# Performance work log

Hardware: AMD Instinct MI355X
Metric: run time of the kernel (lower is better)

## Reference

```python
import jax, jax.numpy as jnp
import numpy as np


def _conv2d(x, w, b, pad, rhs_dilation=(1, 1)):
    out = jax.lax.conv_general_dilated(
        x, w, window_strides=(1, 1),
        padding=((pad, pad), (pad, pad)),
        rhs_dilation=rhs_dilation,
        dimension_numbers=('NCHW', 'OIHW', 'NCHW'))
    return out + b[None, :, None, None]


def _bilinear(img, gx, gy):
    # img [C,H,W]; gx,gy [9,h,w] in [-1,1]; grid_sample bilinear, align_corners=True.
    # Coords are pre-clamped to [-1,1] so all samples are in-bounds; clamped
    # neighbor indices get zero bilinear weight at the boundary, matching torch.
    C, H, W = img.shape
    ix = (gx + 1.0) * 0.5 * (W - 1)
    iy = (gy + 1.0) * 0.5 * (H - 1)
    x0 = jnp.floor(ix)
    y0 = jnp.floor(iy)
    wx = ix - x0
    wy = iy - y0
    x0i = jnp.clip(x0.astype(jnp.int32), 0, W - 1)
    x1i = jnp.clip(x0i + 1, 0, W - 1)
    y0i = jnp.clip(y0.astype(jnp.int32), 0, H - 1)
    y1i = jnp.clip(y0i + 1, 0, H - 1)
    v00 = img[:, y0i, x0i]
    v01 = img[:, y0i, x1i]
    v10 = img[:, y1i, x0i]
    v11 = img[:, y1i, x1i]
    return (v00 * (1 - wx) * (1 - wy) + v01 * wx * (1 - wy)
            + v10 * (1 - wx) * wy + v11 * wx * wy)  # [C,9,h,w]


def _forward(x, conv_w, conv_b, offset_w, offset_b, mod_w, mod_b):
    b, c, h, w = x.shape
    offset = _conv2d(x, offset_w, offset_b, pad=1)          # [b,18,h,w]
    gx = jnp.clip(offset[:, :9] + jnp.linspace(-1.0, 1.0, w)[None, None, None, :], -1.0, 1.0)
    gy = jnp.clip(offset[:, 9:] + jnp.linspace(-1.0, 1.0, h)[None, None, :, None], -1.0, 1.0)
    sampled = jax.vmap(_bilinear)(x, gx, gy)                # [b,c,9,h,w]
    mod = _conv2d(x, mod_w, mod_b, pad=1)                   # [b,9,h,w]
    interp = sampled * mod[:, None]                         # [b,c,9,h,w]
    # tile the 9 samples into a 3h x 3w spatial grid: sample k = i + j*3 goes to block (j, i)
    tiled = interp.reshape(b, c, 3, 3, h, w).transpose(0, 1, 2, 4, 3, 5).reshape(b, c, 3 * h, 3 * w)
    # dilated 3x3 conv with dilation (h+1, w+1), stride 1, padding 1 -> [b,oc,h,w]
    return _conv2d(tiled, conv_w, conv_b, pad=1, rhs_dilation=(h + 1, w + 1))


def setup_inputs() -> dict:
    key = jax.random.key(0)
    ks = jax.random.split(key, 7)
    B, C, OC, H, W = 8, 256, 256, 64, 64
    return {
        'x': jax.random.normal(ks[0], (B, C, H, W), jnp.float32),
        'conv_w': jax.random.normal(ks[1], (OC, C, 3, 3), jnp.float32) * 0.02,
        'conv_b': jax.random.normal(ks[2], (OC,), jnp.float32) * 0.02,
        'offset_w': jax.random.normal(ks[3], (18, C, 3, 3), jnp.float32) * 0.01,
        'offset_b': jax.random.normal(ks[4], (18,), jnp.float32) * 0.01,
        'mod_w': jax.random.normal(ks[5], (9, C, 3, 3), jnp.float32) * 0.02,
        'mod_b': jax.random.normal(ks[6], (9,), jnp.float32) * 0.02,
    }


def reference(x, conv_w, conv_b, offset_w, offset_b, mod_w, mod_b):
    return _forward(x, conv_w, conv_b, offset_w, offset_b, mod_w, mod_b)
```

## Files before the change

### kernel.cpp

```cpp
#include <hip/hip_runtime.h>

typedef __attribute__((ext_vector_type(8))) _Float16 f16x8;
typedef __attribute__((ext_vector_type(4))) float f32x4;

#define CB 8
#define CC 256
#define CHW 4096


__global__ __launch_bounds__(256) void prep_k(const float* __restrict__ convw,
                                              const float* __restrict__ offw,
                                              const float* __restrict__ modw,
                                              _Float16* __restrict__ wAf,
                                              _Float16* __restrict__ wAomF) {
    int i = blockIdx.x * 256 + threadIdx.x;
    {
        int lane = i & 63, tile = (i >> 6) & 15, cc = (i >> 10) & 7, t = i >> 13;
        int oc = tile * 16 + (lane & 15);
        int cb = cc * 32 + (lane >> 4) * 8;
        f16x8 v;
#pragma unroll
        for (int j = 0; j < 8; ++j)
            v[j] = (_Float16)convw[oc * 2304 + (cb + j) * 9 + t];
        *(f16x8*)(wAf + (size_t)i * 8) = v;
    }
    if (i < 9216) {
        int lane = i & 63, tile = (i >> 6) & 1, cc = (i >> 7) & 7, t = i >> 10;
        int mr = tile * 16 + (lane & 15);
        int cb = cc * 32 + (lane >> 4) * 8;
        f16x8 u;
#pragma unroll
        for (int j = 0; j < 8; ++j) {
            int c = cb + j;
            float vv = 0.f;
            if (mr < 18) vv = offw[(mr * 256 + c) * 9 + t];
            else if (mr < 27) vv = modw[((mr - 18) * 256 + c) * 9 + t];
            u[j] = (_Float16)vv;
        }
        *(f16x8*)(wAomF + (size_t)i * 8) = u;
    }
}

__global__ __launch_bounds__(256) void xk(const float* __restrict__ x,
                                          _Float16* __restrict__ xt) {
    __shared__ ushort tile[64][264];
    int bid = blockIdx.x;
    int b = bid & 7, pos0 = (bid >> 3) << 6;
    int tid = threadIdx.x;
    int p = tid & 63;
    const float* xb = x + ((size_t)b << 20);
#pragma unroll 4
    for (int rep = 0; rep < 64; rep++) {
        int c = rep * 4 + (tid >> 6);
        _Float16 h = (_Float16)xb[((size_t)c << 12) + pos0 + p];
        tile[p][c] = __builtin_bit_cast(ushort, h);
    }
    __syncthreads();
    _Float16* xtb = xt + ((size_t)b << 20);
#pragma unroll
    for (int rep = 0; rep < 8; rep++) {
        int item = rep * 256 + tid;
        int pp = item >> 5, ch = item & 31;
        f16x8 v = *(const f16x8*)((const char*)&tile[0][0] + pp * 528 + ch * 16);
        *(f16x8*)((char*)xtb + (((size_t)(pos0 + pp)) << 9) + ch * 16) = v;
    }
}

__global__ __launch_bounds__(256) void k1(const _Float16* __restrict__ xt,
                                          const _Float16* __restrict__ wAomF,
                                          const float* __restrict__ offb,
                                          const float* __restrict__ modb,
                                          float4* __restrict__ descW,
                                          int4* __restrict__ descO) {
    __shared__ float sEp[32][68];

    int bid = blockIdx.x;
    int b = bid & 7, y = bid >> 3;
    int tid = threadIdx.x;
    int lane = tid & 63;
    int w = __builtin_amdgcn_readfirstlane(tid >> 6);
    int l15 = lane & 15, oct = lane >> 4;

    const _Float16* xtb = xt + ((size_t)b << 20);
    int kylo = (y == 0) ? 1 : 0;
    int kyhi = (y == 63) ? 1 : 2;

    f32x4 acc[2];
    acc[0] = (f32x4)0.f;
    acc[1] = (f32x4)0.f;
    f16x8 Z = {};

    int px = (w << 4) + l15;

    for (int ty = kylo; ty <= kyhi; ++ty) {
        int yy = y + ty - 1;
#pragma unroll
        for (int tx = 0; tx < 3; ++tx) {
            int t = ty * 3 + tx;
            int xx = px + tx - 1;
            bool val = (xx >= 0 && xx < 64);
            int xxc = min(max(xx, 0), 63);
            const f16x8* bp = (const f16x8*)(xtb + (((yy << 6) + xxc) << 8) + oct * 8);
            const f16x8* wf = (const f16x8*)wAomF + (size_t)t * 16 * 64 + lane;
#pragma unroll
            for (int c0 = 0; c0 < 256; c0 += 32) {
                f16x8 bf = bp[c0 >> 3];
                if (!val) bf = Z;
                int cc = c0 >> 5;
#pragma unroll
                for (int m = 0; m < 2; m++) {
                    f16x8 af = wf[(cc * 2 + m) * 64];
                    acc[m] = __builtin_amdgcn_mfma_f32_16x16x32_f16(af, bf, acc[m], 0, 0, 0);
                }
            }
        }
    }

#pragma unroll
    for (int m = 0; m < 2; m++) {
#pragma unroll
        for (int r = 0; r < 4; r++) {
            int row = (m << 4) + (oct << 2) + r;
            if (row < 27) sEp[row][px] = acc[m][r];
        }
    }
    __syncthreads();

    int g = tid >> 6;
    int xx2 = tid & 63;
    if (g < 3) {
        float lx = -1.0f + xx2 * (2.0f / 63.0f);
        float ly = -1.0f + y * (2.0f / 63.0f);
#pragma unroll
        for (int j = 0; j < 3; j++) {
            int k = g * 3 + j;
            float gx = sEp[k][xx2] + offb[k] + lx;
            gx = fminf(fmaxf(gx, -1.f), 1.f);
            float gy = sEp[9 + k][xx2] + offb[9 + k] + ly;
            gy = fminf(fmaxf(gy, -1.f), 1.f);
            float m = sEp[18 + k][xx2] + modb[k];
            float ix = (gx + 1.0f) * 0.5f * 63.0f;
            float iy = (gy + 1.0f) * 0.5f * 63.0f;
            float fx = floorf(ix), fy = floorf(iy);
            float wx = ix - fx, wy = iy - fy;
            int x0 = min(max((int)fx, 0), 63);
            int x1 = min(x0 + 1, 63);
            int y0 = min(max((int)fy, 0), 63);
            int y1 = min(y0 + 1, 63);
            float w00 = (1.f - wx) * (1.f - wy) * m;
            float w01 = wx * (1.f - wy) * m;
            float w10 = (1.f - wx) * wy * m;
            float w11 = wx * wy * m;
            int di = ((b * 9 + k) << 12) + (y << 6) + xx2;
            descW[di] = make_float4(w00, w01, w10, w11);
            descO[di] = make_int4(((y0 << 6) + x0) << 9, ((y0 << 6) + x1) << 9,
                                  ((y1 << 6) + x0) << 9, ((y1 << 6) + x1) << 9);
        }
    }
}

__global__ __launch_bounds__(512, 4) void k2(const _Float16* __restrict__ xt,
                                             const _Float16* __restrict__ wAf,
                                             const float4* __restrict__ descW,
                                             const int4* __restrict__ descO,
                                             const float* __restrict__ convb,
                                             float* __restrict__ out) {
    __shared__ char cmb[2][8192];
    __shared__ float4 sDW[2][64];
    __shared__ int sDO[2][256];
    __shared__ f32x4 sred[2048];

    int bid = blockIdx.x;
    int b = bid & 7, oy = bid >> 3;
    int tid = threadIdx.x;
    int l = tid & 63;
    int wid = __builtin_amdgcn_readfirstlane(tid >> 6);
    int mgrp = wid & 3, ks = wid >> 2;
    int oct = l >> 4, l15 = l & 15;

    const char* xtb = (const char*)(xt + ((size_t)b << 20));

    f32x4 acc[4][4];
#pragma unroll
    for (int mt = 0; mt < 4; mt++)
#pragma unroll
        for (int nt = 0; nt < 4; nt++) acc[mt][nt] = (f32x4)0.f;

    int p_ox = (tid >> 3) & 63;
    int p_cs = tid & 7;
    int csl = (p_ox << 7) + ((p_cs ^ (p_ox & 7)) << 4);
    const char* xtb_cs = xtb + p_cs * 16;

    int boff = (l15 << 7) + ((((ks << 2) + oct) ^ (l15 & 7)) << 4);

    auto stage_desc = [&](int t) {
        int slot = t & 1;
        int xx = tid;
        int ky = t / 3, kx = t % 3;
        int yy = oy + ky - 1;
        int xp = xx + kx - 1;
        float4 w4s = make_float4(0.f, 0.f, 0.f, 0.f);
        int4 o4 = make_int4(0, 0, 0, 0);
        if (yy >= 0 && yy < 64 && xp >= 0 && xp < 64) {
            int di = ((b * 9 + t) << 12) + (yy << 6) + xp;
            w4s = descW[di];
            o4 = descO[di];
        }
        sDW[slot][xx] = w4s;
        sDO[slot][xx * 4 + 0] = o4.x;
        sDO[slot][xx * 4 + 1] = o4.y;
        sDO[slot][xx * 4 + 2] = o4.z;
        sDO[slot][xx * 4 + 3] = o4.w;
    };

    int rdo0, rdo1, rdo2, rdo3;
    _Float16 rh0, rh1, rh2, rh3;

    auto refresh_desc = [&](int t) {
        int slot = t & 1;
        const int* dof = &sDO[slot][p_ox * 4];
        rdo0 = dof[0]; rdo1 = dof[1]; rdo2 = dof[2]; rdo3 = dof[3];
        float4 w4 = sDW[slot][p_ox];
        rh0 = (_Float16)w4.x; rh1 = (_Float16)w4.y;
        rh2 = (_Float16)w4.z; rh3 = (_Float16)w4.w;
    };

    f16x8 cr[4];

    auto load_corners = [&](int q) {
        const char* base = xtb_cs + (q << 7);
        cr[0] = *(const f16x8*)(base + rdo0);
        cr[1] = *(const f16x8*)(base + rdo1);
        cr[2] = *(const f16x8*)(base + rdo2);
        cr[3] = *(const f16x8*)(base + rdo3);
    };

    auto write_cmb = [&](int nb) {
        f16x8 W0 = {rh0, rh0, rh0, rh0, rh0, rh0, rh0, rh0};
        f16x8 W1 = {rh1, rh1, rh1, rh1, rh1, rh1, rh1, rh1};
        f16x8 W2 = {rh2, rh2, rh2, rh2, rh2, rh2, rh2, rh2};
        f16x8 W3 = {rh3, rh3, rh3, rh3, rh3, rh3, rh3, rh3};
        f16x8 r = cr[0] * W0 + cr[1] * W1 + cr[2] * W2 + cr[3] * W3;
        *(f16x8*)(cmb[nb] + csl) = r;
    };

    if (tid < 64) stage_desc(0);
    __syncthreads();
    refresh_desc(0);
    load_corners(0);
    write_cmb(0);
    __syncthreads();

    for (int p = 0; p < 36; ++p) {
        int t = p >> 2, q = p & 3, pb = p & 1;
        bool hasNext = (p + 1 < 36);

        f16x8 afr[4];
        {
            const f16x8* wf = (const f16x8*)wAf +
                              ((size_t)((t * 8 + q * 2 + ks) * 16 + mgrp * 4)) * 64 + l;
            afr[0] = wf[0];
            afr[1] = wf[64];
            afr[2] = wf[128];
            afr[3] = wf[192];
        }

        if (hasNext) {
            int pn = p + 1;
            if ((pn & 3) == 0) refresh_desc(pn >> 2);
            load_corners(pn & 3);
        }
        if (q == 0 && t + 1 < 9 && tid < 64) stage_desc(t + 1);

        const char* src = cmb[pb];
        __builtin_amdgcn_s_setprio(1);
        f16x8 bfr[4];
#pragma unroll
        for (int nt = 0; nt < 4; ++nt)
            bfr[nt] = *(const f16x8*)(src + boff + (nt << 11));
#pragma unroll
        for (int nt = 0; nt < 4; ++nt)
#pragma unroll
            for (int mt = 0; mt < 4; ++mt)
                acc[mt][nt] = __builtin_amdgcn_mfma_f32_16x16x32_f16(
                    afr[mt], bfr[nt], acc[mt][nt], 0, 0, 0);
        __builtin_amdgcn_s_setprio(0);

        if (hasNext) write_cmb(pb ^ 1);
        __syncthreads();
    }

#pragma unroll
    for (int R = 0; R < 2; ++R) {
        if (ks == 1) {
#pragma unroll
            for (int mtl = 0; mtl < 2; ++mtl) {
#pragma unroll
                for (int nt = 0; nt < 4; ++nt) {
                    int fi = (((mgrp << 1) + mtl) << 8) + (((nt << 4) + l15) << 2) + oct;
                    sred[fi] = acc[(R << 1) + mtl][nt];
                }
            }
        }
        __syncthreads();
        if (ks == 0) {
#pragma unroll
            for (int mtl = 0; mtl < 2; ++mtl) {
#pragma unroll
                for (int nt = 0; nt < 4; ++nt) {
                    int fi = (((mgrp << 1) + mtl) << 8) + (((nt << 4) + l15) << 2) + oct;
                    acc[(R << 1) + mtl][nt] += sred[fi];
                }
            }
        }
        __syncthreads();
    }

    if (ks == 0) {
        size_t outb = ((size_t)b << 20);
#pragma unroll
        for (int mt = 0; mt < 4; ++mt) {
#pragma unroll
            for (int nt = 0; nt < 4; ++nt) {
                int ox = (nt << 4) + l15;
#pragma unroll
                for (int r = 0; r < 4; ++r) {
                    int oc = (mgrp << 6) + (mt << 4) + (oct << 2) + r;
                    out[outb + (size_t)oc * 4096 + (oy << 6) + ox] = acc[mt][nt][r] + convb[oc];
                }
            }
        }
    }
}

extern "C" void kernel_launch(void* const* d_in, const int* in_sizes, int n_in,
                              void* d_out, int out_size, void* d_ws, size_t ws_size,
                              hipStream_t stream) {
    const float* x     = (const float*)d_in[0];
    const float* convw = (const float*)d_in[1];
    const float* convb = (const float*)d_in[2];
    const float* offw  = (const float*)d_in[3];
    const float* offb  = (const float*)d_in[4];
    const float* modw  = (const float*)d_in[5];
    const float* modb  = (const float*)d_in[6];
    float* out = (float*)d_out;

    char* ws = (char*)d_ws;
    _Float16* wAf   = (_Float16*)(ws);
    _Float16* wAomF = (_Float16*)(ws + 1179648);
    float4*   descW = (float4*)(ws + 1327104);
    int4*     descO = (int4*)(ws + 6045696);
    _Float16* xt    = (_Float16*)(ws + 10764288);

    hipLaunchKernelGGL(prep_k, dim3(288), dim3(256), 0, stream, convw, offw, modw, wAf, wAomF);
    hipLaunchKernelGGL(xk, dim3(512), dim3(256), 0, stream, x, xt);
    hipLaunchKernelGGL(k1, dim3(512), dim3(256), 0, stream, xt, wAomF, offb, modb, descW, descO);
    hipLaunchKernelGGL(k2, dim3(512), dim3(512), 0, stream, xt, wAf, descW, descO, convb, out);
}
```

Baseline: 102.6 us.

## Process two K-chunks per barrier and union LDS buffers in deformable conv kernel

The main loop now handles two 32-channel chunks per iteration (18 iterations instead of 36), with double-buffered pairs of combined-sample tiles in LDS. This halves the number of block barriers. Descriptor staging is split into a register load and a later LDS store so global latency overlaps compute. The final reduction buffer is unioned with the main-loop LDS to keep the footprint down. In exchange the kernel holds more live registers (two A-fragment sets and two corner sets), which may spill or lower occupancy under launch_bounds(512,4). It also swaps __syncthreads for a raw waitcnt+barrier and drops the s_setprio hints.

```diff
diff --git a/kernel.cpp b/kernel.cpp
--- a/kernel.cpp
+++ b/kernel.cpp
@@ -165,10 +165,15 @@
                                              const int4* __restrict__ descO,
                                              const float* __restrict__ convb,
                                              float* __restrict__ out) {
-    __shared__ char cmb[2][8192];
-    __shared__ float4 sDW[2][64];
-    __shared__ int sDO[2][256];
-    __shared__ f32x4 sred[2048];
+    struct Sm {
+        char cmb[2][2][8192];
+        float4 dW[2][64];
+        int4 dO[2][64];
+    };
+    __shared__ union {
+        Sm m;
+        f32x4 sred[2048];
+    } S;
 
     int bid = blockIdx.x;
     int b = bid & 7, oy = bid >> 3;
@@ -193,41 +198,38 @@
 
     int boff = (l15 << 7) + ((((ks << 2) + oct) ^ (l15 & 7)) << 4);
 
-    auto stage_desc = [&](int t) {
-        int slot = t & 1;
-        int xx = tid;
+    float4 dw_reg;
+    int4 do_reg;
+    auto desc_load = [&](int t) {
         int ky = t / 3, kx = t % 3;
         int yy = oy + ky - 1;
-        int xp = xx + kx - 1;
-        float4 w4s = make_float4(0.f, 0.f, 0.f, 0.f);
-        int4 o4 = make_int4(0, 0, 0, 0);
+        int xp = tid + kx - 1;
+        dw_reg = make_float4(0.f, 0.f, 0.f, 0.f);
+        do_reg = make_int4(0, 0, 0, 0);
         if (yy >= 0 && yy < 64 && xp >= 0 && xp < 64) {
             int di = ((b * 9 + t) << 12) + (yy << 6) + xp;
-            w4s = descW[di];
-            o4 = descO[di];
-        }
-        sDW[slot][xx] = w4s;
-        sDO[slot][xx * 4 + 0] = o4.x;
-        sDO[slot][xx * 4 + 1] = o4.y;
-        sDO[slot][xx * 4 + 2] = o4.z;
-        sDO[slot][xx * 4 + 3] = o4.w;
+            dw_reg = descW[di];
+            do_reg = descO[di];
+        }
+    };
+    auto desc_store = [&](int t) {
+        int slot = t & 1;
+        S.m.dW[slot][tid] = dw_reg;
+        S.m.dO[slot][tid] = do_reg;
     };
 
     int rdo0, rdo1, rdo2, rdo3;
     _Float16 rh0, rh1, rh2, rh3;
-
     auto refresh_desc = [&](int t) {
         int slot = t & 1;
-        const int* dof = &sDO[slot][p_ox * 4];
-        rdo0 = dof[0]; rdo1 = dof[1]; rdo2 = dof[2]; rdo3 = dof[3];
-        float4 w4 = sDW[slot][p_ox];
+        int4 o4 = S.m.dO[slot][p_ox];
+        rdo0 = o4.x; rdo1 = o4.y; rdo2 = o4.z; rdo3 = o4.w;
+        float4 w4 = S.m.dW[slot][p_ox];
         rh0 = (_Float16)w4.x; rh1 = (_Float16)w4.y;
         rh2 = (_Float16)w4.z; rh3 = (_Float16)w4.w;
     };
 
-    f16x8 cr[4];
-
-    auto load_corners = [&](int q) {
+    auto issue_q = [&](f16x8* cr, int q) {
         const char* base = xtb_cs + (q << 7);
         cr[0] = *(const f16x8*)(base + rdo0);
         cr[1] = *(const f16x8*)(base + rdo1);
@@ -235,45 +237,26 @@
         cr[3] = *(const f16x8*)(base + rdo3);
     };
 
-    auto write_cmb = [&](int nb) {
+    auto comb_write = [&](const f16x8* cr, char* dst) {
         f16x8 W0 = {rh0, rh0, rh0, rh0, rh0, rh0, rh0, rh0};
         f16x8 W1 = {rh1, rh1, rh1, rh1, rh1, rh1, rh1, rh1};
         f16x8 W2 = {rh2, rh2, rh2, rh2, rh2, rh2, rh2, rh2};
         f16x8 W3 = {rh3, rh3, rh3, rh3, rh3, rh3, rh3, rh3};
         f16x8 r = cr[0] * W0 + cr[1] * W1 + cr[2] * W2 + cr[3] * W3;
-        *(f16x8*)(cmb[nb] + csl) = r;
-    };
-
-    if (tid < 64) stage_desc(0);
-    __syncthreads();
-    refresh_desc(0);
-    load_corners(0);
-    write_cmb(0);
-    __syncthreads();
-
-    for (int p = 0; p < 36; ++p) {
-        int t = p >> 2, q = p & 3, pb = p & 1;
-        bool hasNext = (p + 1 < 36);
-
-        f16x8 afr[4];
-        {
-            const f16x8* wf = (const f16x8*)wAf +
-                              ((size_t)((t * 8 + q * 2 + ks) * 16 + mgrp * 4)) * 64 + l;
-            afr[0] = wf[0];
-            afr[1] = wf[64];
-            afr[2] = wf[128];
-            afr[3] = wf[192];
-        }
-
-        if (hasNext) {
-            int pn = p + 1;
-            if ((pn & 3) == 0) refresh_desc(pn >> 2);
-            load_corners(pn & 3);
-        }
-        if (q == 0 && t + 1 < 9 && tid < 64) stage_desc(t + 1);
-
-        const char* src = cmb[pb];
-        __builtin_amdgcn_s_setprio(1);
+        *(f16x8*)(dst + csl) = r;
+    };
+
+    auto load_afr = [&](f16x8* afr, int m) {
+        int t = m >> 2, q = m & 3;
+        const f16x8* wf = (const f16x8*)wAf +
+                          ((size_t)((t * 8 + q * 2 + ks) * 16 + mgrp * 4)) * 64 + l;
+        afr[0] = wf[0];
+        afr[1] = wf[64];
+        afr[2] = wf[128];
+        afr[3] = wf[192];
+    };
+
+    auto do_mfma = [&](const char* src, const f16x8* afr) {
         f16x8 bfr[4];
 #pragma unroll
         for (int nt = 0; nt < 4; ++nt)
@@ -284,12 +267,60 @@
             for (int mt = 0; mt < 4; ++mt)
                 acc[mt][nt] = __builtin_amdgcn_mfma_f32_16x16x32_f16(
                     afr[mt], bfr[nt], acc[mt][nt], 0, 0, 0);
-        __builtin_amdgcn_s_setprio(0);
-
-        if (hasNext) write_cmb(pb ^ 1);
-        __syncthreads();
-    }
-
+    };
+
+    if (tid < 64) {
+        desc_load(0);
+        desc_store(0);
+        desc_load(1);
+    }
+    __syncthreads();
+    refresh_desc(0);
+    {
+        f16x8 c0[4], c1[4];
+        issue_q(c0, 0);
+        issue_q(c1, 1);
+        comb_write(c0, S.m.cmb[0][0]);
+        comb_write(c1, S.m.cmb[0][1]);
+    }
+    __syncthreads();
+
+#pragma unroll 2
+    for (int P = 0; P < 18; ++P) {
+        int ma = 2 * P, pb = P & 1;
+        bool more = (P < 17);
+
+        f16x8 afrA[4], afrB[4];
+        load_afr(afrA, ma);
+        load_afr(afrB, ma + 1);
+
+        if (P & 1) {
+            int T = (P + 1) >> 1;
+            refresh_desc(T);
+            if (T + 1 <= 8 && tid < 64) desc_load(T + 1);
+        } else {
+            int Ts = (P >> 1) + 1;
+            if (Ts <= 8 && tid < 64) desc_store(Ts);
+        }
+
+        f16x8 crA[4], crB[4];
+        if (more) issue_q(crA, (ma + 2) & 3);
+
+        do_mfma(S.m.cmb[pb][0], afrA);
+
+        if (more) {
+            issue_q(crB, (ma + 3) & 3);
+            comb_write(crA, S.m.cmb[pb ^ 1][0]);
+        }
+
+        do_mfma(S.m.cmb[pb][1], afrB);
+
+        if (more) comb_write(crB, S.m.cmb[pb ^ 1][1]);
+
+        asm volatile("s_waitcnt lgkmcnt(0)\n\ts_barrier" ::: "memory");
+    }
+
+    __syncthreads();
 #pragma unroll
     for (int R = 0; R < 2; ++R) {
         if (ks == 1) {
@@ -298,7 +329,7 @@
 #pragma unroll
                 for (int nt = 0; nt < 4; ++nt) {
                     int fi = (((mgrp << 1) + mtl) << 8) + (((nt << 4) + l15) << 2) + oct;
-                    sred[fi] = acc[(R << 1) + mtl][nt];
+                    S.sred[fi] = acc[(R << 1) + mtl][nt];
                 }
             }
         }
@@ -309,7 +340,7 @@
 #pragma unroll
                 for (int nt = 0; nt < 4; ++nt) {
                     int fi = (((mgrp << 1) + mtl) << 8) + (((nt << 4) + l15) << 2) + oct;
-                    acc[(R << 1) + mtl][nt] += sred[fi];
+                    acc[(R << 1) + mtl][nt] += S.sred[fi];
                 }
             }
         }
```

Measured after the change: 272.5 us. +165.6%, slower.

## Process two K-chunks per barrier and union LDS buffers in deformable conv kernel

Applied to the files above, without the earlier changes.

Restructures the main MFMA loop so that each iteration handles two channel quarters, using double-buffered pairs of combined-sample tiles. This halves the number of block-wide barriers. The LDS reduction scratch is unioned with the main-loop buffers so the larger tile storage does not raise shared memory use much. The descriptor offsets are now stored as int4 for vector LDS access, and the wave priority hints are removed.

```diff
diff --git a/kernel.cpp b/kernel.cpp
--- a/kernel.cpp
+++ b/kernel.cpp
@@ -159,16 +159,21 @@
     }
 }
 
+struct SmK2 {
+    char cmb[2][2][8192];
+    float4 dW[2][64];
+    int4 dO[2][64];
+};
 __global__ __launch_bounds__(512, 4) void k2(const _Float16* __restrict__ xt,
                                              const _Float16* __restrict__ wAf,
                                              const float4* __restrict__ descW,
                                              const int4* __restrict__ descO,
                                              const float* __restrict__ convb,
                                              float* __restrict__ out) {
-    __shared__ char cmb[2][8192];
-    __shared__ float4 sDW[2][64];
-    __shared__ int sDO[2][256];
-    __shared__ f32x4 sred[2048];
+    __shared__ union SU {
+        SmK2 m;
+        f32x4 sred[2048];
+    } S;
 
     int bid = blockIdx.x;
     int b = bid & 7, oy = bid >> 3;
@@ -206,28 +211,22 @@
             w4s = descW[di];
             o4 = descO[di];
         }
-        sDW[slot][xx] = w4s;
-        sDO[slot][xx * 4 + 0] = o4.x;
-        sDO[slot][xx * 4 + 1] = o4.y;
-        sDO[slot][xx * 4 + 2] = o4.z;
-        sDO[slot][xx * 4 + 3] = o4.w;
+        S.m.dW[slot][xx] = w4s;
+        S.m.dO[slot][xx] = o4;
     };
 
     int rdo0, rdo1, rdo2, rdo3;
     _Float16 rh0, rh1, rh2, rh3;
-
     auto refresh_desc = [&](int t) {
         int slot = t & 1;
-        const int* dof = &sDO[slot][p_ox * 4];
-        rdo0 = dof[0]; rdo1 = dof[1]; rdo2 = dof[2]; rdo3 = dof[3];
-        float4 w4 = sDW[slot][p_ox];
+        int4 o4 = S.m.dO[slot][p_ox];
+        rdo0 = o4.x; rdo1 = o4.y; rdo2 = o4.z; rdo3 = o4.w;
+        float4 w4 = S.m.dW[slot][p_ox];
         rh0 = (_Float16)w4.x; rh1 = (_Float16)w4.y;
         rh2 = (_Float16)w4.z; rh3 = (_Float16)w4.w;
     };
 
-    f16x8 cr[4];
-
-    auto load_corners = [&](int q) {
+    auto issue_q = [&](f16x8* cr, int q) {
         const char* base = xtb_cs + (q << 7);
         cr[0] = *(const f16x8*)(base + rdo0);
         cr[1] = *(const f16x8*)(base + rdo1);
@@ -235,58 +234,74 @@
         cr[3] = *(const f16x8*)(base + rdo3);
     };
 
-    auto write_cmb = [&](int nb) {
+    auto comb_write = [&](const f16x8* cr, char* dst) {
         f16x8 W0 = {rh0, rh0, rh0, rh0, rh0, rh0, rh0, rh0};
         f16x8 W1 = {rh1, rh1, rh1, rh1, rh1, rh1, rh1, rh1};
         f16x8 W2 = {rh2, rh2, rh2, rh2, rh2, rh2, rh2, rh2};
         f16x8 W3 = {rh3, rh3, rh3, rh3, rh3, rh3, rh3, rh3};
         f16x8 r = cr[0] * W0 + cr[1] * W1 + cr[2] * W2 + cr[3] * W3;
-        *(f16x8*)(cmb[nb] + csl) = r;
+        *(f16x8*)(dst + csl) = r;
+    };
+
+    auto load_afr = [&](f16x8* afr, int m) {
+        int t = m >> 2, q = m & 3;
+        const f16x8* wf = (const f16x8*)wAf +
+                          ((size_t)((t * 8 + q * 2 + ks) * 16 + mgrp * 4)) * 64 + l;
+        afr[0] = wf[0];
+        afr[1] = wf[64];
+        afr[2] = wf[128];
+        afr[3] = wf[192];
+    };
+
+    auto do_mfma = [&](const char* src, const f16x8* afr) {
+        f16x8 bfr[4];
+#pragma unroll
+        for (int nt = 0; nt < 4; ++nt)
+            bfr[nt] = *(const f16x8*)(src + boff + (nt << 11));
+#pragma unroll
+        for (int nt = 0; nt < 4; ++nt)
+#pragma unroll
+            for (int mt = 0; mt < 4; ++mt)
+                acc[mt][nt] = __builtin_amdgcn_mfma_f32_16x16x32_f16(
+                    afr[mt], bfr[nt], acc[mt][nt], 0, 0, 0);
     };
 
     if (tid < 64) stage_desc(0);
     __syncthreads();
     refresh_desc(0);
-    load_corners(0);
-    write_cmb(0);
+    {
+        f16x8 c0[4];
+        issue_q(c0, 0);
+        comb_write(c0, S.m.cmb[0][0]);
+        issue_q(c0, 1);
+        comb_write(c0, S.m.cmb[0][1]);
+    }
     __syncthreads();
 
-    for (int p = 0; p < 36; ++p) {
-        int t = p >> 2, q = p & 3, pb = p & 1;
-        bool hasNext = (p + 1 < 36);
+    for (int P = 0; P < 18; ++P) {
+        int pb = P & 1;
+        int t = P >> 1;
+        bool more = (P < 17);
+
+        if (!(P & 1)) {
+            if (t + 1 <= 8 && tid < 64) stage_desc(t + 1);
+        } else if (more) {
+            refresh_desc((P + 1) >> 1);
+        }
 
         f16x8 afr[4];
-        {
-            const f16x8* wf = (const f16x8*)wAf +
-                              ((size_t)((t * 8 + q * 2 + ks) * 16 + mgrp * 4)) * 64 + l;
-            afr[0] = wf[0];
-            afr[1] = wf[64];
-            afr[2] = wf[128];
-            afr[3] = wf[192];
-        }
-
-        if (hasNext) {
-            int pn = p + 1;
-            if ((pn & 3) == 0) refresh_desc(pn >> 2);
-            load_corners(pn & 3);
-        }
-        if (q == 0 && t + 1 < 9 && tid < 64) stage_desc(t + 1);
-
-        const char* src = cmb[pb];
-        __builtin_amdgcn_s_setprio(1);
-        f16x8 bfr[4];
-#pragma unroll
-        for (int nt = 0; nt < 4; ++nt)
-            bfr[nt] = *(const f16x8*)(src + boff + (nt << 11));
-#pragma unroll
-        for (int nt = 0; nt < 4; ++nt)
-#pragma unroll
-            for (int mt = 0; mt < 4; ++mt)
-                acc[mt][nt] = __builtin_amdgcn_mfma_f32_16x16x32_f16(
-                    afr[mt], bfr[nt], acc[mt][nt], 0, 0, 0);
-        __builtin_amdgcn_s_setprio(0);
-
-        if (hasNext) write_cmb(pb ^ 1);
+        f16x8 cr[4];
+
+        load_afr(afr, 2 * P);
+        if (more) issue_q(cr, (2 * P + 2) & 3);
+        do_mfma(S.m.cmb[pb][0], afr);
+        load_afr(afr, 2 * P + 1);
+        if (more) comb_write(cr, S.m.cmb[pb ^ 1][0]);
+
+        if (more) issue_q(cr, (2 * P + 3) & 3);
+        do_mfma(S.m.cmb[pb][1], afr);
+        if (more) comb_write(cr, S.m.cmb[pb ^ 1][1]);
+
         __syncthreads();
     }
 
@@ -298,7 +313,7 @@
 #pragma unroll
                 for (int nt = 0; nt < 4; ++nt) {
                     int fi = (((mgrp << 1) + mtl) << 8) + (((nt << 4) + l15) << 2) + oct;
-                    sred[fi] = acc[(R << 1) + mtl][nt];
+                    S.sred[fi] = acc[(R << 1) + mtl][nt];
                 }
             }
         }
@@ -309,7 +324,7 @@
 #pragma unroll
                 for (int nt = 0; nt < 4; ++nt) {
                     int fi = (((mgrp << 1) + mtl) << 8) + (((nt << 4) + l15) << 2) + oct;
-                    acc[(R << 1) + mtl][nt] += sred[fi];
+                    acc[(R << 1) + mtl][nt] += S.sred[fi];
                 }
             }
         }
```

Result: no change. 103.1 us (+0.5%).
